# Kernel optimization log

Measured on AMD Instinct MI355X. Metric: run time of the kernel, lower is better.

## Reference

```python
import jax, jax.numpy as jnp
import numpy as np

# Supernet configuration (matches init_kwargs)
HIDDEN = [1024, 2048]
HEADS = [8, 16]
ABITS = [4, 8]
WBITS = [4, 8]
B, S = 4, 4096
MAX_IN = max(HIDDEN)            # 2048
MAX_OUT = max(HIDDEN)           # min(heads)*max(hidden)//min(heads) = 2048


def fake_quant(v, s, bit):
    """LSQ-style symmetric fake quantization with straight-through rounding."""
    qp = float(2 ** (bit - 1) - 1)
    qn = -float(2 ** (bit - 1))
    vs = jnp.clip(v / s, qn, qp)
    vq = vs + jax.lax.stop_gradient(jnp.round(vs) - vs)  # STE round
    return vq * s


def setup_inputs() -> dict:
    key = jax.random.key(0)
    k1, k2, k3, k4 = jax.random.split(key, 4)
    x = jax.random.normal(k1, (B, S, MAX_IN), jnp.float32)
    weights = jax.random.uniform(k2, (16,), jnp.float32)  # arch mixing coeffs
    W = jax.random.normal(k3, (MAX_OUT, MAX_IN), jnp.float32) * 0.02
    b = jax.random.normal(k4, (MAX_OUT,), jnp.float32) * 0.02
    # init_weight_scale: LSQ init 2*mean(|W|)/sqrt(Qp) per weight bitwidth
    w_scales = jnp.stack([2.0 * jnp.mean(jnp.abs(W)) / jnp.sqrt(float(2 ** (bit - 1) - 1))
                          for bit in WBITS])
    a_scales = jnp.ones((len(ABITS),), jnp.float32)
    return {"x": x, "weights": weights, "W": W, "b": b,
            "a_scales": a_scales, "w_scales": w_scales}


def reference(x, weights, W, b, a_scales, w_scales):
    # Non-argmax mixture path (reverse=False):
    # for each (hidden_i, heads_j, abit_m, wbit_n): slice W to
    # [out_dim, in_dim], zero-pad to [MAX_OUT, MAX_IN] (== masking, since
    # per-tensor fake-quant maps 0 -> 0), quantize, and weighted-accumulate.
    # Quantized x / W depend only on abit / wbit, so compute each once.
    qx = [fake_quant(x, a_scales[m], ABITS[m]) for m in range(len(ABITS))]   # [B,S,MAX_IN]
    qw = [fake_quant(W, w_scales[n], WBITS[n]) for n in range(len(WBITS))]  # [MAX_OUT,MAX_IN]
    out_idx = jnp.arange(MAX_OUT)
    in_idx = jnp.arange(MAX_IN)

    w_mix = jnp.zeros_like(W)
    x_mix = jnp.zeros_like(x)
    b_mix = jnp.zeros_like(b)
    k = 0
    for i, h in enumerate(HIDDEN):
        for j, nh in enumerate(HEADS):
            head_dim = h // nh
            out_dim = nh * head_dim  # == h when divisible
            in_dim = h
            wmask = (out_idx[:, None] < out_dim) & (in_idx[None, :] < in_dim)
            bmask = out_idx < out_dim
            for m in range(len(ABITS)):
                for n in range(len(WBITS)):
                    a = weights[k]
                    w_mix = w_mix + a * jnp.where(wmask, qw[n], 0.0)
                    x_mix = x_mix + a * qx[m]
                    b_mix = b_mix + a * jnp.where(bmask, b, 0.0)
                    k += 1
    # out = F.linear(x_mix, w_mix, b_mix)
    out = jnp.einsum('bsi,oi->bso', x_mix, w_mix) + b_mix
    return out
```

## Files before the change

kernel.cpp:

```cpp
#include <hip/hip_runtime.h>
#include <hip/hip_bf16.h>
#include <stdint.h>

#define MDIM 16384
#define NDIM 2048
#define KDIM 2048

typedef __attribute__((ext_vector_type(4))) float f32x4;
typedef __attribute__((ext_vector_type(8))) short s16x8;

__device__ __forceinline__ void gload_lds16(const __hip_bfloat16* g, void* l) {
    __builtin_amdgcn_global_load_lds(
        (const __attribute__((address_space(1))) void*)g,
        (__attribute__((address_space(3))) void*)l,
        16, 0, 0);
}


__global__ __launch_bounds__(256) void prep_x(
    const float* __restrict__ x, const float* __restrict__ weights,
    const float* __restrict__ a_scales, __hip_bfloat16* __restrict__ xq)
{
    float A0 = 0.f, A1 = 0.f;
    #pragma unroll
    for (int k = 0; k < 16; ++k) {
        float w = weights[k];
        if (((k >> 1) & 1) == 0) A0 += w; else A1 += w;
    }
    const float s0 = a_scales[0], s1 = a_scales[1];
    const float r0 = 1.f / s0, r1 = 1.f / s1;

    size_t idx = ((size_t)blockIdx.x * 256 + threadIdx.x) * 8;
    const f32x4* xv = (const f32x4*)(x + idx);
    f32x4 v0 = xv[0], v1 = xv[1];
    float vals[8] = {v0.x, v0.y, v0.z, v0.w, v1.x, v1.y, v1.z, v1.w};

    union { s16x8 v; __hip_bfloat16 h[8]; } u;
    #pragma unroll
    for (int j = 0; j < 8; ++j) {
        float q0 = rintf(fminf(fmaxf(vals[j] * r0, -8.f),   7.f)) * s0;
        float q1 = rintf(fminf(fmaxf(vals[j] * r1, -128.f), 127.f)) * s1;
        u.h[j] = __float2bfloat16(A0 * q0 + A1 * q1);
    }
    *(s16x8*)(xq + idx) = u.v;
}

__global__ __launch_bounds__(256) void prep_w(
    const float* __restrict__ W, const float* __restrict__ weights,
    const float* __restrict__ w_scales, __hip_bfloat16* __restrict__ wq)
{
    float c00 = weights[0] + weights[2]  + weights[4]  + weights[6];
    float c01 = weights[1] + weights[3]  + weights[5]  + weights[7];
    float c10 = weights[8] + weights[10] + weights[12] + weights[14];
    float c11 = weights[9] + weights[11] + weights[13] + weights[15];

    const float s0 = w_scales[0], s1 = w_scales[1];
    const float r0 = 1.f / s0, r1 = 1.f / s1;

    size_t idx = ((size_t)blockIdx.x * 256 + threadIdx.x) * 8;
    const int o = (int)(idx >> 11);
    const int c = (int)(idx & 2047);
    const bool inner = (o < 1024) && (c < 1024);
    const float k0 = inner ? (c00 + c10) : c10;
    const float k1 = inner ? (c01 + c11) : c11;

    const f32x4* wv = (const f32x4*)(W + idx);
    f32x4 v0 = wv[0], v1 = wv[1];
    float vals[8] = {v0.x, v0.y, v0.z, v0.w, v1.x, v1.y, v1.z, v1.w};

    union { s16x8 v; __hip_bfloat16 h[8]; } u;
    #pragma unroll
    for (int j = 0; j < 8; ++j) {
        float q0 = rintf(fminf(fmaxf(vals[j] * r0, -8.f),   7.f)) * s0;
        float q1 = rintf(fminf(fmaxf(vals[j] * r1, -128.f), 127.f)) * s1;
        u.h[j] = __float2bfloat16(k0 * q0 + k1 * q1);
    }
    *(s16x8*)(wq + idx) = u.v;
}

__global__ __launch_bounds__(256) void prep_b(
    const float* __restrict__ b, const float* __restrict__ weights,
    float* __restrict__ bm)
{
    int o = blockIdx.x * 256 + threadIdx.x;
    if (o >= NDIM) return;
    float S1 = 0.f, S0 = 0.f;
    #pragma unroll
    for (int k = 0; k < 8; ++k)  S0 += weights[k];
    #pragma unroll
    for (int k = 8; k < 16; ++k) S1 += weights[k];
    bm[o] = b[o] * ((o < 1024) ? (S0 + S1) : S1);
}


#define BM 256
#define BN 256
#define NCH 64
#define SLOTB 32768

#define MFMA(a, b, c) __builtin_amdgcn_mfma_f32_16x16x32_bf16((a), (b), (c), 0, 0, 0)

#define CHUNK(S, T)                                                          \
  {                                                                          \
                                                      \
    _Pragma("unroll")                                                        \
    for (int m_ = 0; m_ < 8; ++m_)                                           \
      af[m_] = *(const s16x8*)(lds + (S) * SLOTB + aoff + m_ * 1024);        \
    bf[0] = *(const s16x8*)(lds + (S) * SLOTB + 16384 + boff);               \
    bf[1] = *(const s16x8*)(lds + (S) * SLOTB + 16384 + boff + 1024);        \
    gload_lds16(As0 + kg * 32, lds + (T) * SLOTB + ldoff);                   \
    gload_lds16(As1 + kg * 32, lds + (T) * SLOTB + 8192 + ldoff);            \
    __builtin_amdgcn_s_barrier();                                            \
    asm volatile("s_waitcnt lgkmcnt(0)" ::: "memory");                       \
    __builtin_amdgcn_sched_barrier(0);                                       \
    __builtin_amdgcn_s_setprio(1);                                           \
    _Pragma("unroll")                                                        \
    for (int m_ = 0; m_ < 8; ++m_) {                                         \
      acc[m_][0] = MFMA(af[m_], bf[0], acc[m_][0]);                          \
      acc[m_][1] = MFMA(af[m_], bf[1], acc[m_][1]);                          \
    }                                                                        \
    __builtin_amdgcn_s_setprio(0);                                           \
    __builtin_amdgcn_s_barrier();                                            \
                                                      \
    bf[2] = *(const s16x8*)(lds + (S) * SLOTB + 16384 + boff + 2048);        \
    bf[3] = *(const s16x8*)(lds + (S) * SLOTB + 16384 + boff + 3072);        \
    gload_lds16(Bs0 + kg * 32, lds + (T) * SLOTB + 16384 + ldoff);           \
    gload_lds16(Bs1 + kg * 32, lds + (T) * SLOTB + 24576 + ldoff);           \
    asm volatile("s_waitcnt vmcnt(8)" ::: "memory");                         \
    __builtin_amdgcn_s_barrier();                                            \
    asm volatile("s_waitcnt lgkmcnt(0)" ::: "memory");                       \
    __builtin_amdgcn_sched_barrier(0);                                       \
    __builtin_amdgcn_s_setprio(1);                                           \
    _Pragma("unroll")                                                        \
    for (int m_ = 0; m_ < 8; ++m_) {                                         \
      acc[m_][2] = MFMA(af[m_], bf[2], acc[m_][2]);                          \
      acc[m_][3] = MFMA(af[m_], bf[3], acc[m_][3]);                          \
    }                                                                        \
    __builtin_amdgcn_s_setprio(0);                                           \
    __builtin_amdgcn_s_barrier();                                            \
    kg = (kg + 1) & (NCH - 1);                                               \
  }

__global__ __launch_bounds__(512, 2) void gemm256(
    const __hip_bfloat16* __restrict__ A,
    const __hip_bfloat16* __restrict__ B,
    const float* __restrict__ bias,
    float* __restrict__ C)
{
    __shared__ char lds[4 * SLOTB];

    const int tid  = threadIdx.x;
    const int lane = tid & 63;
    const int wid  = tid >> 6;
    const int wm   = wid >> 2;
    const int wn   = wid & 3;

    const int bid  = blockIdx.x;
    const int swz  = (bid & 7) * 64 + (bid >> 3);
    const int brow = (swz >> 3) * BM;
    const int bcol = (swz & 7) * BN;

    const int csw = (tid & 3) ^ ((tid >> 3) & 3);
    const __hip_bfloat16* As0 = A + (size_t)(brow + (tid >> 2)) * KDIM + csw * 8;
    const __hip_bfloat16* As1 = As0 + (size_t)128 * KDIM;
    const __hip_bfloat16* Bs0 = B + (size_t)(bcol + (tid >> 2)) * KDIM + csw * 8;
    const __hip_bfloat16* Bs1 = Bs0 + (size_t)128 * KDIM;
    const int ldoff = tid * 16;

    const int fr  = lane & 15;
    const int l16 = lane >> 4;
    const int xr  = (l16 ^ ((fr >> 1) & 3)) * 16;
    const int aoff = (wm * 128 + fr) * 64 + xr;
    const int boff = (wn * 64  + fr) * 64 + xr;

    f32x4 acc[8][4];
    #pragma unroll
    for (int m = 0; m < 8; ++m)
        #pragma unroll
        for (int n = 0; n < 4; ++n)
            acc[m][n] = (f32x4){0.f, 0.f, 0.f, 0.f};

    s16x8 af[8], bf[4];
    int kg = 3;

    #pragma unroll
    for (int q = 0; q < 3; ++q) {
        gload_lds16(As0 + q * 32, lds + q * SLOTB + ldoff);
        gload_lds16(As1 + q * 32, lds + q * SLOTB +  8192 + ldoff);
        gload_lds16(Bs0 + q * 32, lds + q * SLOTB + 16384 + ldoff);
        gload_lds16(Bs1 + q * 32, lds + q * SLOTB + 24576 + ldoff);
    }
    asm volatile("s_waitcnt vmcnt(8)" ::: "memory");
    __builtin_amdgcn_s_barrier();

    #pragma unroll 1
    for (int it = 0; it < NCH / 4; ++it) {
        CHUNK(0, 3);
        CHUNK(1, 0);
        CHUNK(2, 1);
        CHUNK(3, 2);
    }
    asm volatile("s_waitcnt vmcnt(0) lgkmcnt(0)" ::: "memory");

    const int ccol0 = bcol + wn * 64 + fr;
    const int crow0 = brow + wm * 128 + l16 * 4;
    float bv[4];
    #pragma unroll
    for (int n = 0; n < 4; ++n) bv[n] = bias[ccol0 + n * 16];

    #pragma unroll
    for (int m = 0; m < 8; ++m) {
        #pragma unroll
        for (int j = 0; j < 4; ++j) {
            float* Crow = C + (size_t)(crow0 + m * 16 + j) * NDIM;
            #pragma unroll
            for (int n = 0; n < 4; ++n)
                Crow[ccol0 + n * 16] = acc[m][n][j] + bv[n];
        }
    }
}


extern "C" void kernel_launch(void* const* d_in, const int* in_sizes, int n_in,
                              void* d_out, int out_size, void* d_ws, size_t ws_size,
                              hipStream_t stream) {
    const float* x        = (const float*)d_in[0];
    const float* weights  = (const float*)d_in[1];
    const float* W        = (const float*)d_in[2];
    const float* b        = (const float*)d_in[3];
    const float* a_scales = (const float*)d_in[4];
    const float* w_scales = (const float*)d_in[5];
    float* out = (float*)d_out;

    __hip_bfloat16* xq = (__hip_bfloat16*)d_ws;
    __hip_bfloat16* wq = (__hip_bfloat16*)((char*)d_ws + 67108864);
    float*          bm = (float*)((char*)d_ws + 67108864 + 8388608);

    prep_w<<<dim3((NDIM * KDIM) / (256 * 8)), dim3(256), 0, stream>>>(W, weights, w_scales, wq);
    prep_b<<<dim3(NDIM / 256), dim3(256), 0, stream>>>(b, weights, bm);
    prep_x<<<dim3(((size_t)MDIM * KDIM) / (256 * 8)), dim3(256), 0, stream>>>(x, weights, a_scales, xq);
    gemm256<<<dim3((MDIM / BM) * (NDIM / BN)), dim3(512), 0, stream>>>(xq, wq, bm, out);
}
```

Baseline: 166.0 us.

## Merge two half-chunk phases into one with a single barrier per K-chunk

Restructures the GEMM main loop so each K-chunk loads all A and B fragments from LDS up front, issues all four global-to-LDS prefetches together, and runs all 32 MFMAs in one phase. This removes three of the four s_barriers and the explicit lgkmcnt waits per chunk, leaving the compiler to schedule the LDS-read waits. LDS is reorganised into separate A and B regions (same total size). The tradeoff is less fine-grained interleaving of memory and compute, and more live fragment registers at once.

```diff
diff --git a/kernel.cpp b/kernel.cpp
--- a/kernel.cpp
+++ b/kernel.cpp
@@ -96,49 +96,37 @@
 #define BM 256
 #define BN 256
 #define NCH 64
-#define SLOTB 32768
+#define ASLOT 16384
+#define BREG  65536
 
 #define MFMA(a, b, c) __builtin_amdgcn_mfma_f32_16x16x32_bf16((a), (b), (c), 0, 0, 0)
 
 #define CHUNK(S, T)                                                          \
   {                                                                          \
-                                                      \
+    asm volatile("" ::: "memory");      \
+    s16x8 af[8], bf[4];                                                      \
     _Pragma("unroll")                                                        \
     for (int m_ = 0; m_ < 8; ++m_)                                           \
-      af[m_] = *(const s16x8*)(lds + (S) * SLOTB + aoff + m_ * 1024);        \
-    bf[0] = *(const s16x8*)(lds + (S) * SLOTB + 16384 + boff);               \
-    bf[1] = *(const s16x8*)(lds + (S) * SLOTB + 16384 + boff + 1024);        \
-    gload_lds16(As0 + kg * 32, lds + (T) * SLOTB + ldoff);                   \
-    gload_lds16(As1 + kg * 32, lds + (T) * SLOTB + 8192 + ldoff);            \
-    __builtin_amdgcn_s_barrier();                                            \
-    asm volatile("s_waitcnt lgkmcnt(0)" ::: "memory");                       \
-    __builtin_amdgcn_sched_barrier(0);                                       \
+      af[m_] = *(const s16x8*)(lds + (S) * ASLOT + aoff + m_ * 1024);        \
+    _Pragma("unroll")                                                        \
+    for (int n_ = 0; n_ < 4; ++n_)                                           \
+      bf[n_] = *(const s16x8*)(lds + BREG + (S) * ASLOT + boff + n_ * 1024); \
+    gload_lds16(As0 + kg * 32, lds + (T) * ASLOT + ldoff);                   \
+    gload_lds16(As1 + kg * 32, lds + (T) * ASLOT + 8192 + ldoff);            \
+    gload_lds16(Bs0 + kg * 32, lds + BREG + (T) * ASLOT + ldoff);            \
+    gload_lds16(Bs1 + kg * 32, lds + BREG + (T) * ASLOT + 8192 + ldoff);     \
+    kg = (kg + 1) & (NCH - 1);                                               \
     __builtin_amdgcn_s_setprio(1);                                           \
     _Pragma("unroll")                                                        \
     for (int m_ = 0; m_ < 8; ++m_) {                                         \
       acc[m_][0] = MFMA(af[m_], bf[0], acc[m_][0]);                          \
       acc[m_][1] = MFMA(af[m_], bf[1], acc[m_][1]);                          \
-    }                                                                        \
-    __builtin_amdgcn_s_setprio(0);                                           \
-    __builtin_amdgcn_s_barrier();                                            \
-                                                      \
-    bf[2] = *(const s16x8*)(lds + (S) * SLOTB + 16384 + boff + 2048);        \
-    bf[3] = *(const s16x8*)(lds + (S) * SLOTB + 16384 + boff + 3072);        \
-    gload_lds16(Bs0 + kg * 32, lds + (T) * SLOTB + 16384 + ldoff);           \
-    gload_lds16(Bs1 + kg * 32, lds + (T) * SLOTB + 24576 + ldoff);           \
-    asm volatile("s_waitcnt vmcnt(8)" ::: "memory");                         \
-    __builtin_amdgcn_s_barrier();                                            \
-    asm volatile("s_waitcnt lgkmcnt(0)" ::: "memory");                       \
-    __builtin_amdgcn_sched_barrier(0);                                       \
-    __builtin_amdgcn_s_setprio(1);                                           \
-    _Pragma("unroll")                                                        \
-    for (int m_ = 0; m_ < 8; ++m_) {                                         \
       acc[m_][2] = MFMA(af[m_], bf[2], acc[m_][2]);                          \
       acc[m_][3] = MFMA(af[m_], bf[3], acc[m_][3]);                          \
     }                                                                        \
     __builtin_amdgcn_s_setprio(0);                                           \
+    asm volatile("s_waitcnt vmcnt(8)" ::: "memory");   \
     __builtin_amdgcn_s_barrier();                                            \
-    kg = (kg + 1) & (NCH - 1);                                               \
   }
 
 __global__ __launch_bounds__(512, 2) void gemm256(
@@ -147,7 +135,7 @@
     const float* __restrict__ bias,
     float* __restrict__ C)
 {
-    __shared__ char lds[4 * SLOTB];
+    __shared__ char lds[8 * ASLOT];
 
     const int tid  = threadIdx.x;
     const int lane = tid & 63;
@@ -180,15 +168,14 @@
         for (int n = 0; n < 4; ++n)
             acc[m][n] = (f32x4){0.f, 0.f, 0.f, 0.f};
 
-    s16x8 af[8], bf[4];
     int kg = 3;
 
     #pragma unroll
     for (int q = 0; q < 3; ++q) {
-        gload_lds16(As0 + q * 32, lds + q * SLOTB + ldoff);
-        gload_lds16(As1 + q * 32, lds + q * SLOTB +  8192 + ldoff);
-        gload_lds16(Bs0 + q * 32, lds + q * SLOTB + 16384 + ldoff);
-        gload_lds16(Bs1 + q * 32, lds + q * SLOTB + 24576 + ldoff);
+        gload_lds16(As0 + q * 32, lds + q * ASLOT + ldoff);
+        gload_lds16(As1 + q * 32, lds + q * ASLOT + 8192 + ldoff);
+        gload_lds16(Bs0 + q * 32, lds + BREG + q * ASLOT + ldoff);
+        gload_lds16(Bs1 + q * 32, lds + BREG + q * ASLOT + 8192 + ldoff);
     }
     asm volatile("s_waitcnt vmcnt(8)" ::: "memory");
     __builtin_amdgcn_s_barrier();
```

Result: faster. 162.5 us (-2.1%).
